# Kernel tuning notes

Hardware: AMD Instinct MI355X
Metric: run time of the kernel (lower is better)

## Reference

```python
import jax, jax.numpy as jnp
import numpy as np
import math

B, S, E, H = 2, 2048, 768, 12
D = E // H            # head_dim = 64
FFN = 3072            # GeGLU hidden
WIN = 64              # local window size
GLOBAL_IDS = np.array([0])
EPS = 1e-5


def _rope(x):
    # x: [B,H,S,D]; interleaved rotary embedding, theta=10000 (lucidrains RotaryEmbedding)
    d = x.shape[-1]
    s = x.shape[-2]
    inv_freq = 1.0 / (10000.0 ** (jnp.arange(0, d, 2, dtype=jnp.float32) / d))
    freqs = jnp.arange(s, dtype=jnp.float32)[:, None] * inv_freq[None, :]  # [S, D/2]
    freqs = jnp.repeat(freqs, 2, axis=-1)                                   # [S, D]
    cos, sin = jnp.cos(freqs), jnp.sin(freqs)
    xp = x.reshape(x.shape[:-1] + (d // 2, 2))
    x_rot = jnp.stack([-xp[..., 1], xp[..., 0]], axis=-1).reshape(x.shape)
    return x * cos + x_rot * sin


def _layernorm(x, scale, bias):
    mu = jnp.mean(x, axis=-1, keepdims=True)
    var = jnp.mean(jnp.square(x - mu), axis=-1, keepdims=True)
    return (x - mu) * jax.lax.rsqrt(var + EPS) * scale + bias


def setup_inputs() -> dict:
    key = jax.random.key(0)
    ks = jax.random.split(key, 10)
    def xav(k, shape, gain):
        fan_out, fan_in = shape
        std = gain * math.sqrt(2.0 / (fan_in + fan_out))
        return jax.random.normal(k, shape, jnp.float32) * std
    g2 = math.sqrt(2.0)
    g13 = math.sqrt(1.0 / 3.0)
    return {
        "x": jax.random.normal(ks[0], (B, S, E), jnp.float32),
        "rel_pos_bias": jax.random.normal(ks[1], (B, S, S), jnp.float32),
        "mask": jnp.ones((B, S), dtype=bool),
        "wq_w": xav(ks[2], (E, E), g2), "wq_b": jnp.zeros((E,), jnp.float32),
        "wk_w": xav(ks[3], (E, E), g2), "wk_b": jnp.zeros((E,), jnp.float32),
        "wv_w": xav(ks[4], (E, E), g2), "wv_b": jnp.zeros((E,), jnp.float32),
        "fc_w": xav(ks[5], (E, E), g2), "fc_b": jnp.zeros((E,), jnp.float32),
        "pos_coeff": jnp.full((H, 1, 1), 0.01, jnp.float32),
        "gate_w": xav(ks[6], (FFN, E), g13), "gate_b": jnp.zeros((FFN,), jnp.float32),
        "value_w": xav(ks[7], (FFN, E), g2), "value_b": jnp.zeros((FFN,), jnp.float32),
        "down_w": xav(ks[8], (E, FFN), g2), "down_b": jnp.zeros((E,), jnp.float32),
        "ln1_s": jnp.ones((E,), jnp.float32), "ln1_b": jnp.zeros((E,), jnp.float32),
        "ln2_s": jnp.ones((E,), jnp.float32), "ln2_b": jnp.zeros((E,), jnp.float32),
    }


def _sparse_allow(mask):
    # static local-window + global-token pattern, [S,S] bool
    idx = jnp.arange(S)
    allow = jnp.abs(idx[:, None] - idx[None, :]) <= WIN
    gidx = jnp.asarray(GLOBAL_IDS)
    allow = allow.at[gidx, :].set(True)
    allow = allow.at[:, gidx].set(True)
    # combine with padding mask [B,S] broadcast over query rows
    return allow[None, None, :, :] & mask[:, None, None, :]  # [B,1,S,S]


def reference(x, rel_pos_bias, mask, wq_w, wq_b, wk_w, wk_b, wv_w, wv_b,
              fc_w, fc_b, pos_coeff, gate_w, gate_b, value_w, value_b,
              down_w, down_b, ln1_s, ln1_b, ln2_s, ln2_b):
    def heads(t):  # [B,S,E] -> [B,H,S,D]
        return t.reshape(B, S, H, D).transpose(0, 2, 1, 3)

    Q = _rope(heads(x @ wq_w.T + wq_b))
    K = _rope(heads(x @ wk_w.T + wk_b))
    V = heads(x @ wv_w.T + wv_b)

    scores = jnp.einsum('bhqd,bhkd->bhqk', Q, K) / math.sqrt(D)
    scores = scores + pos_coeff[None] * rel_pos_bias[:, None]     # [B,H,S,S]
    allow = _sparse_allow(mask)
    scores = jnp.where(allow, scores, -1e30)
    scores = scores - jnp.max(scores, axis=-1, keepdims=True)
    attn = jax.nn.softmax(scores, axis=-1)
    ctx = jnp.einsum('bhqk,bhkd->bhqd', attn, V)
    ctx = ctx.transpose(0, 2, 1, 3).reshape(B, S, E)
    attn_out = ctx @ fc_w.T + fc_b

    h = _layernorm(x + attn_out, ln1_s, ln1_b)
    gate = jax.nn.gelu(h @ gate_w.T + gate_b, approximate=False)
    ffn = (gate * (h @ value_w.T + value_b)) @ down_w.T + down_b
    return _layernorm(h + ffn, ln2_s, ln2_b)
```

## Files before the change

kernel.cpp:

```cpp
#include <hip/hip_runtime.h>
#include <math.h>

#define B_   2
#define S_   2048
#define E_   768
#define H_   12
#define D_   64
#define FFN_ 3072
#define WIN_ 64
#define MTOT (B_*S_)

typedef unsigned short ushort_t;
typedef unsigned short ushort8 __attribute__((ext_vector_type(8)));
typedef __bf16 bf16x8 __attribute__((ext_vector_type(8)));
typedef float f32x4 __attribute__((ext_vector_type(4)));
typedef _Float16 half_t;

__device__ __forceinline__ float b2f(ushort_t u) {
    union { unsigned int i; float f; } c; c.i = ((unsigned int)u) << 16; return c.f;
}
__device__ __forceinline__ ushort_t f2b(float f) {
    union { float f; unsigned int i; } c; c.f = f;
    unsigned int u = c.i;
    return (ushort_t)((u + 0x7fffu + ((u >> 16) & 1u)) >> 16);
}
__device__ __forceinline__ float gelu_f(float g) {
    return 0.5f * g * (1.f + erff(g * 0.70710678118654752440f));
}

typedef const __attribute__((address_space(1))) void* gptr_t;
typedef __attribute__((address_space(3))) void* lptr_t;
__device__ __forceinline__ void gload16(const void* g, void* l) {
    __builtin_amdgcn_global_load_lds((gptr_t)g,
        (lptr_t)(unsigned int)(unsigned long long)l, 16, 0, 0);
}

__global__ __launch_bounds__(256)
void cvt_f32_bf16(const float* __restrict__ in, ushort_t* __restrict__ out, int n8)
{
    const int idx = blockIdx.x * 256 + threadIdx.x;
    if (idx >= n8) return;
    const float4* p = (const float4*)(in + (size_t)idx * 8);
    const float4 a = p[0], b = p[1];
    ushort8 o;
    o[0]=f2b(a.x); o[1]=f2b(a.y); o[2]=f2b(a.z); o[3]=f2b(a.w);
    o[4]=f2b(b.x); o[5]=f2b(b.y); o[6]=f2b(b.z); o[7]=f2b(b.w);
    *(ushort8*)(out + (size_t)idx*8) = o;
}

__global__ __launch_bounds__(256)
void cvt_interleave(const float* __restrict__ gw, const float* __restrict__ vw,
                    ushort_t* __restrict__ out)
{
    const int idx = blockIdx.x*256 + threadIdx.x;
    const int R   = idx / 96, c8 = idx - R*96;
    const int blk = R >> 6, w = R & 63;
    const float* src = (w < 32 ? gw : vw) + (size_t)(blk*32 + (w & 31))*768 + c8*8;
    const float4 a = ((const float4*)src)[0], b = ((const float4*)src)[1];
    ushort8 o;
    o[0]=f2b(a.x); o[1]=f2b(a.y); o[2]=f2b(a.z); o[3]=f2b(a.w);
    o[4]=f2b(b.x); o[5]=f2b(b.y); o[6]=f2b(b.z); o[7]=f2b(b.w);
    *(ushort8*)(out + (size_t)idx*8) = o;
}

__global__ __launch_bounds__(256)
void rope_table(float2* __restrict__ ctab)
{
    const int idx = blockIdx.x*256 + threadIdx.x;
    if (idx >= S_*32) return;
    const int s = idx >> 5, i = idx & 31;
    const float inv = exp2f(-(float)i * (13.287712379549449f/32.0f));
    const float fr = (float)s * inv;
    ctab[idx] = make_float2(cosf(fr), sinf(fr));
}

__global__ __launch_bounds__(256)
void rope_apply(ushort_t* __restrict__ Qb, ushort_t* __restrict__ Kb,
                const float2* __restrict__ ctab)
{
    const int NP4 = MTOT*E_/8;
    int idx = blockIdx.x*256 + threadIdx.x;
    ushort_t* ptr = Qb;
    if (idx >= NP4) { ptr = Kb; idx -= NP4; if (idx >= NP4) return; }
    const size_t p0 = (size_t)idx * 4;
    const int e2 = (int)(p0 % (E_/2));
    const int s  = (int)((p0 / (E_/2)) % S_);
    const int i0 = e2 & 31;
    ushort8 v = *(ushort8*)(ptr + p0*2);
    ushort8 o;
#pragma unroll
    for (int t = 0; t < 4; ++t) {
        const float2 cs = ctab[s*32 + i0 + t];
        const float x0 = b2f(v[2*t]), x1 = b2f(v[2*t+1]);
        o[2*t]   = f2b(x0*cs.x - x1*cs.y);
        o[2*t+1] = f2b(x1*cs.x + x0*cs.y);
    }
    *(ushort8*)(ptr + p0*2) = o;
}

template<int EPI, int BN>
__global__ __launch_bounds__(256)
void gemm_mfma(const ushort_t* __restrict__ A,
               const ushort_t* W0, const float* b0, void* C0,
               const ushort_t* W1, const float* b1, void* C1,
               const ushort_t* W2, const float* b2, void* C2,
               const void* __restrict__ aux, int M, int N, int K)
{
    constexpr int NWC = BN/64, NWR = 4/NWC, WROWS = 128/NWR, MF = WROWS/16;
    const ushort_t* W = W0; const float* bias = b0; void* C = C0;
    if (blockIdx.z == 1) { W = W1; bias = b1; C = C1; }
    else if (blockIdx.z == 2) { W = W2; bias = b2; C = C2; }

    __shared__ __align__(16) ushort_t As[128*32];
    __shared__ __align__(16) ushort_t Bs[BN*32];

    const int tid = threadIdx.x, wv = tid>>6, lane = tid&63;
    const int m0 = blockIdx.y*128, n0 = blockIdx.x*BN;
    const int wr = wv / NWC, wc = wv % NWC;
    const int lr16 = lane & 15, lkb = (lane>>4)<<3;

    f32x4 acc[MF][4];
#pragma unroll
    for (int i=0;i<MF;++i)
#pragma unroll
        for (int j=0;j<4;++j) acc[i][j] = f32x4{0.f,0.f,0.f,0.f};

    const char* Ab = (const char*)(A + (size_t)m0*K);
    const char* Wb = (const char*)(W + (size_t)n0*K);
    const size_t rb = (size_t)K*2;
    const int wbase = wv*1024, lby = lane*16;

    for (int kt = 0; kt < K; kt += 32) {
        const size_t kb = (size_t)kt*2;
        int n_ = wbase + lby;
        gload16(Ab + (size_t)(n_>>6)*rb + kb + (n_&63), (char*)As + wbase);
        n_ += 4096;
        gload16(Ab + (size_t)(n_>>6)*rb + kb + (n_&63), (char*)As + wbase + 4096);
        n_ = wbase + lby;
        gload16(Wb + (size_t)(n_>>6)*rb + kb + (n_&63), (char*)Bs + wbase);
        if (BN == 128) {
            n_ += 4096;
            gload16(Wb + (size_t)(n_>>6)*rb + kb + (n_&63), (char*)Bs + wbase + 4096);
        }
        __syncthreads();
        bf16x8 af[MF], bfr[4];
#pragma unroll
        for (int mf=0; mf<MF; ++mf)
            af[mf] = *(const bf16x8*)&As[(wr*WROWS + mf*16 + lr16)*32 + lkb];
#pragma unroll
        for (int nf=0; nf<4; ++nf)
            bfr[nf] = *(const bf16x8*)&Bs[(wc*64 + nf*16 + lr16)*32 + lkb];
#pragma unroll
        for (int mf=0; mf<MF; ++mf)
#pragma unroll
            for (int nf=0; nf<4; ++nf)
                acc[mf][nf] = __builtin_amdgcn_mfma_f32_16x16x32_bf16(af[mf], bfr[nf], acc[mf][nf], 0,0,0);
        __syncthreads();
    }

    const int colb = n0 + wc*64 + lr16;
    const int rowb = m0 + wr*WROWS + ((lane>>4)<<2);
#pragma unroll
    for (int nf=0; nf<4; ++nf) {
        const int col = colb + nf*16;
        const float bsv = bias[col];
#pragma unroll
        for (int mf=0; mf<MF; ++mf) {
            const int row = rowb + mf*16;
            const f32x4 a = acc[mf][nf];
#pragma unroll
            for (int r=0; r<4; ++r) {
                const size_t off = (size_t)(row+r)*N + col;
                const float v = a[r] + bsv;
                if constexpr (EPI == 0) {
                    ((ushort_t*)C)[off] = f2b(v);
                } else if constexpr (EPI == 1) {
                    ((float*)C)[off] = v + ((const float*)aux)[off];
                } else {
                    if (blockIdx.z == 2) {
                        const int rr = row + r;
                        const size_t toff =
                            (((size_t)(rr >> 11)*H_ + (col >> 6))*64 + (col & 63))*(size_t)S_ + (rr & (S_-1));
                        ((ushort_t*)C)[toff] = f2b(v);
                    } else {
                        ((ushort_t*)C)[off] = f2b(v);
                    }
                }
            }
        }
    }
}

__global__ __launch_bounds__(256, 2)
void gemm_geglu(const ushort_t* __restrict__ A,
                const ushort_t* __restrict__ Wgv,
                const float* __restrict__ bgp,
                const float* __restrict__ bvp,
                ushort_t* __restrict__ C)
{
    constexpr int NT   = 12;
    constexpr int ABY  = 128*128;
    constexpr int BUFB = 2*ABY;
    __shared__ __align__(16) char lds[2*BUFB];

    const int id  = blockIdx.x;
    const int stI = (id & 7)*3 + ((id >> 3) >> 6);
    const int w64 = (id >> 3) & 63;
    const int gy  = (stI/6)*8 + (w64 >> 3);
    const int gx  = (stI%6)*8 + (w64 & 7);
    const int m0 = gy*128, n0 = gx*128;

    const int tid = threadIdx.x, wv = tid>>6, l = tid&63;
    const int wr = wv>>1, wc = wv&1;
    const int lr16 = l & 15, g16b = (l>>4)<<4;
    const int xr = (lr16 & 7) << 4;

    const int lrow = l >> 3;
    const int swzc = ((l & 7) ^ lrow) << 4;
    const char* Agp = (const char*)A   + (size_t)(m0 + wv*32 + lrow)*1536 + swzc;
    const char* Bgp = (const char*)Wgv + (size_t)(n0 + wv*32 + lrow)*1536 + swzc;

    const int rA0 = (wr*64 +  0 + lr16)*128, rA1 = (wr*64 + 16 + lr16)*128;
    const int rA2 = (wr*64 + 32 + lr16)*128, rA3 = (wr*64 + 48 + lr16)*128;
    const int rB0 = ABY + (wc*64 +  0 + lr16)*128, rB1 = ABY + (wc*64 + 16 + lr16)*128;
    const int rB2 = ABY + (wc*64 + 32 + lr16)*128, rB3 = ABY + (wc*64 + 48 + lr16)*128;
    const int ck0 = g16b ^ xr, ck1 = (64 + g16b) ^ xr;

    f32x4 acc[4][4];
#pragma unroll
    for (int i=0;i<4;++i)
#pragma unroll
        for (int j=0;j<4;++j) acc[i][j] = f32x4{0.f,0.f,0.f,0.f};

#define STG(tt, cb) { \
    char* dA = lds + (cb)*BUFB + wv*4096; \
    char* dB = lds + (cb)*BUFB + ABY + wv*4096; \
    const size_t ko = (size_t)(tt)*128; \
    gload16(Agp + ko,           dA); \
    gload16(Agp + ko +  8*1536, dA + 1024); \
    gload16(Agp + ko + 16*1536, dA + 2048); \
    gload16(Agp + ko + 24*1536, dA + 3072); \
    gload16(Bgp + ko,           dB); \
    gload16(Bgp + ko +  8*1536, dB + 1024); \
    gload16(Bgp + ko + 16*1536, dB + 2048); \
    gload16(Bgp + ko + 24*1536, dB + 3072); }

    STG(0, 0);
    __syncthreads();

    int c = 0;
#pragma unroll 1
    for (int t = 0; t < NT; ++t) {
        if (t < NT-1) STG(t+1, c^1);
        const char* Lb = lds + c*BUFB;
        const bf16x8 a0 = *(const bf16x8*)(Lb + rA0 + ck0);
        const bf16x8 a1 = *(const bf16x8*)(Lb + rA1 + ck0);
        const bf16x8 a2 = *(const bf16x8*)(Lb + rA2 + ck0);
        const bf16x8 a3 = *(const bf16x8*)(Lb + rA3 + ck0);
        const bf16x8 b0 = *(const bf16x8*)(Lb + rB0 + ck0);
        const bf16x8 b1 = *(const bf16x8*)(Lb + rB1 + ck0);
        const bf16x8 b2 = *(const bf16x8*)(Lb + rB2 + ck0);
        const bf16x8 b3 = *(const bf16x8*)(Lb + rB3 + ck0);
        const bf16x8 e0 = *(const bf16x8*)(Lb + rA0 + ck1);
        const bf16x8 e1 = *(const bf16x8*)(Lb + rA1 + ck1);
        const bf16x8 e2 = *(const bf16x8*)(Lb + rA2 + ck1);
        const bf16x8 e3 = *(const bf16x8*)(Lb + rA3 + ck1);
        const bf16x8 f0 = *(const bf16x8*)(Lb + rB0 + ck1);
        const bf16x8 f1 = *(const bf16x8*)(Lb + rB1 + ck1);
        const bf16x8 f2 = *(const bf16x8*)(Lb + rB2 + ck1);
        const bf16x8 f3 = *(const bf16x8*)(Lb + rB3 + ck1);
        __builtin_amdgcn_s_setprio(1);
        acc[0][0] = __builtin_amdgcn_mfma_f32_16x16x32_bf16(a0, b0, acc[0][0], 0,0,0);
        acc[1][0] = __builtin_amdgcn_mfma_f32_16x16x32_bf16(a1, b0, acc[1][0], 0,0,0);
        acc[2][0] = __builtin_amdgcn_mfma_f32_16x16x32_bf16(a2, b0, acc[2][0], 0,0,0);
        acc[3][0] = __builtin_amdgcn_mfma_f32_16x16x32_bf16(a3, b0, acc[3][0], 0,0,0);
        acc[0][1] = __builtin_amdgcn_mfma_f32_16x16x32_bf16(a0, b1, acc[0][1], 0,0,0);
        acc[1][1] = __builtin_amdgcn_mfma_f32_16x16x32_bf16(a1, b1, acc[1][1], 0,0,0);
        acc[2][1] = __builtin_amdgcn_mfma_f32_16x16x32_bf16(a2, b1, acc[2][1], 0,0,0);
        acc[3][1] = __builtin_amdgcn_mfma_f32_16x16x32_bf16(a3, b1, acc[3][1], 0,0,0);
        acc[0][2] = __builtin_amdgcn_mfma_f32_16x16x32_bf16(a0, b2, acc[0][2], 0,0,0);
        acc[1][2] = __builtin_amdgcn_mfma_f32_16x16x32_bf16(a1, b2, acc[1][2], 0,0,0);
        acc[2][2] = __builtin_amdgcn_mfma_f32_16x16x32_bf16(a2, b2, acc[2][2], 0,0,0);
        acc[3][2] = __builtin_amdgcn_mfma_f32_16x16x32_bf16(a3, b2, acc[3][2], 0,0,0);
        acc[0][3] = __builtin_amdgcn_mfma_f32_16x16x32_bf16(a0, b3, acc[0][3], 0,0,0);
        acc[1][3] = __builtin_amdgcn_mfma_f32_16x16x32_bf16(a1, b3, acc[1][3], 0,0,0);
        acc[2][3] = __builtin_amdgcn_mfma_f32_16x16x32_bf16(a2, b3, acc[2][3], 0,0,0);
        acc[3][3] = __builtin_amdgcn_mfma_f32_16x16x32_bf16(a3, b3, acc[3][3], 0,0,0);
        acc[0][0] = __builtin_amdgcn_mfma_f32_16x16x32_bf16(e0, f0, acc[0][0], 0,0,0);
        acc[1][0] = __builtin_amdgcn_mfma_f32_16x16x32_bf16(e1, f0, acc[1][0], 0,0,0);
        acc[2][0] = __builtin_amdgcn_mfma_f32_16x16x32_bf16(e2, f0, acc[2][0], 0,0,0);
        acc[3][0] = __builtin_amdgcn_mfma_f32_16x16x32_bf16(e3, f0, acc[3][0], 0,0,0);
        acc[0][1] = __builtin_amdgcn_mfma_f32_16x16x32_bf16(e0, f1, acc[0][1], 0,0,0);
        acc[1][1] = __builtin_amdgcn_mfma_f32_16x16x32_bf16(e1, f1, acc[1][1], 0,0,0);
        acc[2][1] = __builtin_amdgcn_mfma_f32_16x16x32_bf16(e2, f1, acc[2][1], 0,0,0);
        acc[3][1] = __builtin_amdgcn_mfma_f32_16x16x32_bf16(e3, f1, acc[3][1], 0,0,0);
        acc[0][2] = __builtin_amdgcn_mfma_f32_16x16x32_bf16(e0, f2, acc[0][2], 0,0,0);
        acc[1][2] = __builtin_amdgcn_mfma_f32_16x16x32_bf16(e1, f2, acc[1][2], 0,0,0);
        acc[2][2] = __builtin_amdgcn_mfma_f32_16x16x32_bf16(e2, f2, acc[2][2], 0,0,0);
        acc[3][2] = __builtin_amdgcn_mfma_f32_16x16x32_bf16(e3, f2, acc[3][2], 0,0,0);
        acc[0][3] = __builtin_amdgcn_mfma_f32_16x16x32_bf16(e0, f3, acc[0][3], 0,0,0);
        acc[1][3] = __builtin_amdgcn_mfma_f32_16x16x32_bf16(e1, f3, acc[1][3], 0,0,0);
        acc[2][3] = __builtin_amdgcn_mfma_f32_16x16x32_bf16(e2, f3, acc[2][3], 0,0,0);
        acc[3][3] = __builtin_amdgcn_mfma_f32_16x16x32_bf16(e3, f3, acc[3][3], 0,0,0);
        __builtin_amdgcn_s_setprio(0);
        __syncthreads();
        c ^= 1;
    }
#undef STG

    const int colb = gx*64 + wc*32 + lr16;
    const int rowb = m0 + wr*64 + ((l>>4)<<2);
#pragma unroll
    for (int nf=0; nf<2; ++nf) {
        const int col = colb + nf*16;
        const float bgv = bgp[col], bvv = bvp[col];
#pragma unroll
        for (int mf=0; mf<4; ++mf) {
            const int row = rowb + mf*16;
            const f32x4 gq = acc[mf][nf];
            const f32x4 vq = acc[mf][nf+2];
#pragma unroll
            for (int r=0; r<4; ++r) {
                C[(size_t)(row+r)*3072 + col] =
                    f2b(gelu_f(gq[r] + bgv) * (vq[r] + bvv));
            }
        }
    }
}

__global__ __launch_bounds__(256, 3)
void gemm_down(const ushort_t* __restrict__ A,
               const ushort_t* __restrict__ Wd,
               const float* __restrict__ bias,
               float* __restrict__ P0,
               half_t* __restrict__ P1)
{
    constexpr int NT   = 24;
    constexpr int ABY  = 128*128;
    constexpr int BBY  = 64*128;
    constexpr int BUFB = ABY + BBY;
    __shared__ __align__(16) char lds[2*BUFB];

    const int id   = blockIdx.x;
    const int work = (id & 7)*96 + (id >> 3);
    const int z    = work / 384;
    const int r    = work - z*384;
    const int gy   = r / 12, gx = r - gy*12;
    const int m0 = gy*128, n0 = gx*64;

    const int tid = threadIdx.x, wv = tid>>6, l = tid&63;
    const int wr = wv>>1, wc = wv&1;
    const int lr16 = l & 15, g16b = (l>>4)<<4;
    const int xr = (lr16 & 7) << 4;

    const int lrow = l >> 3;
    const int swzc = ((l & 7) ^ lrow) << 4;
    const size_t kbase = (size_t)z*3072;
    const char* Agp = (const char*)A  + (size_t)(m0 + wv*32 + lrow)*6144 + kbase + swzc;
    const char* Bgp = (const char*)Wd + (size_t)(n0 + wv*16 + lrow)*6144 + kbase + swzc;

    const int rA0 = (wr*64 +  0 + lr16)*128, rA1 = (wr*64 + 16 + lr16)*128;
    const int rA2 = (wr*64 + 32 + lr16)*128, rA3 = (wr*64 + 48 + lr16)*128;
    const int rB0 = ABY + (wc*32 +  0 + lr16)*128;
    const int rB1 = ABY + (wc*32 + 16 + lr16)*128;
    const int ck0 = g16b ^ xr, ck1 = (64 + g16b) ^ xr;

    f32x4 acc[4][2];
#pragma unroll
    for (int i=0;i<4;++i)
#pragma unroll
        for (int j=0;j<2;++j) acc[i][j] = f32x4{0.f,0.f,0.f,0.f};

#define STGD(tt, cb) { \
    char* dA = lds + (cb)*BUFB + wv*4096; \
    char* dB = lds + (cb)*BUFB + ABY + wv*2048; \
    const size_t ko = (size_t)(tt)*128; \
    gload16(Agp + ko,           dA); \
    gload16(Agp + ko +  8*6144, dA + 1024); \
    gload16(Agp + ko + 16*6144, dA + 2048); \
    gload16(Agp + ko + 24*6144, dA + 3072); \
    gload16(Bgp + ko,           dB); \
    gload16(Bgp + ko +  8*6144, dB + 1024); }

    STGD(0, 0);
    __syncthreads();

    int c = 0;
#pragma unroll 1
    for (int t = 0; t < NT; ++t) {
        if (t < NT-1) STGD(t+1, c^1);
        const char* Lb = lds + c*BUFB;
        const bf16x8 a0 = *(const bf16x8*)(Lb + rA0 + ck0);
        const bf16x8 a1 = *(const bf16x8*)(Lb + rA1 + ck0);
        const bf16x8 a2 = *(const bf16x8*)(Lb + rA2 + ck0);
        const bf16x8 a3 = *(const bf16x8*)(Lb + rA3 + ck0);
        const bf16x8 b0 = *(const bf16x8*)(Lb + rB0 + ck0);
        const bf16x8 b1 = *(const bf16x8*)(Lb + rB1 + ck0);
        const bf16x8 e0 = *(const bf16x8*)(Lb + rA0 + ck1);
        const bf16x8 e1 = *(const bf16x8*)(Lb + rA1 + ck1);
        const bf16x8 e2 = *(const bf16x8*)(Lb + rA2 + ck1);
        const bf16x8 e3 = *(const bf16x8*)(Lb + rA3 + ck1);
        const bf16x8 f0 = *(const bf16x8*)(Lb + rB0 + ck1);
        const bf16x8 f1 = *(const bf16x8*)(Lb + rB1 + ck1);
        __builtin_amdgcn_s_setprio(1);
        acc[0][0] = __builtin_amdgcn_mfma_f32_16x16x32_bf16(a0, b0, acc[0][0], 0,0,0);
        acc[1][0] = __builtin_amdgcn_mfma_f32_16x16x32_bf16(a1, b0, acc[1][0], 0,0,0);
        acc[2][0] = __builtin_amdgcn_mfma_f32_16x16x32_bf16(a2, b0, acc[2][0], 0,0,0);
        acc[3][0] = __builtin_amdgcn_mfma_f32_16x16x32_bf16(a3, b0, acc[3][0], 0,0,0);
        acc[0][1] = __builtin_amdgcn_mfma_f32_16x16x32_bf16(a0, b1, acc[0][1], 0,0,0);
        acc[1][1] = __builtin_amdgcn_mfma_f32_16x16x32_bf16(a1, b1, acc[1][1], 0,0,0);
        acc[2][1] = __builtin_amdgcn_mfma_f32_16x16x32_bf16(a2, b1, acc[2][1], 0,0,0);
        acc[3][1] = __builtin_amdgcn_mfma_f32_16x16x32_bf16(a3, b1, acc[3][1], 0,0,0);
        acc[0][0] = __builtin_amdgcn_mfma_f32_16x16x32_bf16(e0, f0, acc[0][0], 0,0,0);
        acc[1][0] = __builtin_amdgcn_mfma_f32_16x16x32_bf16(e1, f0, acc[1][0], 0,0,0);
        acc[2][0] = __builtin_amdgcn_mfma_f32_16x16x32_bf16(e2, f0, acc[2][0], 0,0,0);
        acc[3][0] = __builtin_amdgcn_mfma_f32_16x16x32_bf16(e3, f0, acc[3][0], 0,0,0);
        acc[0][1] = __builtin_amdgcn_mfma_f32_16x16x32_bf16(e0, f1, acc[0][1], 0,0,0);
        acc[1][1] = __builtin_amdgcn_mfma_f32_16x16x32_bf16(e1, f1, acc[1][1], 0,0,0);
        acc[2][1] = __builtin_amdgcn_mfma_f32_16x16x32_bf16(e2, f1, acc[2][1], 0,0,0);
        acc[3][1] = __builtin_amdgcn_mfma_f32_16x16x32_bf16(e3, f1, acc[3][1], 0,0,0);
        __builtin_amdgcn_s_setprio(0);
        __syncthreads();
        c ^= 1;
    }
#undef STGD

    const int colb = n0 + wc*32 + lr16;
    const int rowb = m0 + wr*64 + ((l>>4)<<2);
#pragma unroll
    for (int nf=0; nf<2; ++nf) {
        const int col = colb + nf*16;
        const float bsv = bias[col];
#pragma unroll
        for (int mf=0; mf<4; ++mf) {
            const int row = rowb + mf*16;
            const f32x4 a = acc[mf][nf];
#pragma unroll
            for (int rr=0; rr<4; ++rr) {
                const size_t off = (size_t)(row+rr)*E_ + col;
                if (z == 0) P0[off] = a[rr] + bsv;
                else        P1[off] = (half_t)a[rr];
            }
        }
    }
}

__global__ __launch_bounds__(256)
void attn_mfma(const ushort_t* __restrict__ Qb, const ushort_t* __restrict__ Kb,
               const ushort_t* __restrict__ Vt, const float* __restrict__ rel,
               const float* __restrict__ pos_coeff, ushort_t* __restrict__ ctx)
{
    __shared__ __align__(16) ushort_t P_lds[4][16][160];
    const int id = blockIdx.x;
    const int h  = id % H_;
    const int qb = (id / H_) & 31;
    const int b  = id / (H_*32);
    const int wv = threadIdx.x >> 6, l = threadIdx.x & 63;
    const int qw = qb*64 + wv*16;
    const int g  = l >> 4, ql = l & 15;
    const int q  = qw + ql;

    int klo = qw - 64;
    if (klo < 0) klo = 0;
    if (klo > S_-160) klo = S_-160;
    const bool addg = (klo > 0);
    const float pc = pos_coeff[h];

    const ushort_t* qbp = Qb + ((size_t)(b*S_ + qw))*E_ + h*D_ + (size_t)ql*E_ + g*8;
    const bf16x8 qf0 = *(const bf16x8*)(qbp);
    const bf16x8 qf1 = *(const bf16x8*)(qbp + 32);

    float sg = -1e30f, pg = 0.f;
    const float* relrow = rel + ((size_t)(b*S_ + q))*S_;
    if (addg) {
        const ushort_t* k0p = Kb + (size_t)(b*S_)*E_ + h*D_ + g*8;
        const bf16x8 k00 = *(const bf16x8*)(k0p);
        const bf16x8 k01 = *(const bf16x8*)(k0p + 32);
        float part = 0.f;
#pragma unroll
        for (int t = 0; t < 8; ++t) {
            part = fmaf((float)k00[t], (float)qf0[t], part);
            part = fmaf((float)k01[t], (float)qf1[t], part);
        }
        part += __shfl_xor(part, 16);
        part += __shfl_xor(part, 32);
        sg = part*0.125f + pc*relrow[0];
    }

    f32x4 sc_[10];
#pragma unroll
    for (int f = 0; f < 10; ++f) sc_[f] = f32x4{0.f,0.f,0.f,0.f};
    const ushort_t* kbp = Kb + ((size_t)(b*S_ + klo))*E_ + h*D_;
#pragma unroll
    for (int f = 0; f < 10; ++f) {
        const ushort_t* kr = kbp + (size_t)(16*f + ql)*E_ + g*8;
        const bf16x8 kf0 = *(const bf16x8*)(kr);
        const bf16x8 kf1 = *(const bf16x8*)(kr + 32);
        sc_[f] = __builtin_amdgcn_mfma_f32_16x16x32_bf16(kf0, qf0, sc_[f], 0,0,0);
        sc_[f] = __builtin_amdgcn_mfma_f32_16x16x32_bf16(kf1, qf1, sc_[f], 0,0,0);
    }

#pragma unroll
    for (int f = 0; f < 10; ++f) {
#pragma unroll
        for (int r = 0; r < 4; ++r) {
            const int slot = 16*f + 4*g + r;
            const int key  = klo + slot;
            const int dd   = key - q;
            const bool ok  = (dd <= WIN_ && dd >= -WIN_) || (key == 0);
            const float v  = sc_[f][r]*0.125f + pc*relrow[key];
            sc_[f][r] = ok ? v : -1e30f;
        }
    }

    float mx = sg;
#pragma unroll
    for (int f = 0; f < 10; ++f)
#pragma unroll
        for (int r = 0; r < 4; ++r) mx = fmaxf(mx, sc_[f][r]);
    mx = fmaxf(mx, __shfl_xor(mx, 16));
    mx = fmaxf(mx, __shfl_xor(mx, 32));

    float ls = 0.f;
#pragma unroll
    for (int f = 0; f < 10; ++f)
#pragma unroll
        for (int r = 0; r < 4; ++r) {
            const float p = __expf(sc_[f][r] - mx);
            sc_[f][r] = p; ls += p;
        }
    if (addg) pg = __expf(sg - mx);
    ls += (g == 0) ? pg : 0.f;
    ls += __shfl_xor(ls, 16);
    ls += __shfl_xor(ls, 32);
    const float inv = 1.f / ls;

#pragma unroll
    for (int f = 0; f < 10; ++f)
#pragma unroll
        for (int r = 0; r < 4; ++r)
            P_lds[wv][ql][16*f + 4*g + r] = f2b(sc_[f][r]);
    __syncthreads();

    f32x4 acc_c[4];
#pragma unroll
    for (int df = 0; df < 4; ++df) acc_c[df] = f32x4{0.f,0.f,0.f,0.f};
    const ushort_t* vtb = Vt + ((size_t)(b*H_ + h)*64)*(size_t)S_;
#pragma unroll
    for (int s5 = 0; s5 < 5; ++s5) {
        const bf16x8 pf = *(const bf16x8*)&P_lds[wv][ql][32*s5 + 8*g];
#pragma unroll
        for (int df = 0; df < 4; ++df) {
            const bf16x8 vtf = *(const bf16x8*)(vtb + (size_t)(df*16 + ql)*S_ + klo + 32*s5 + g*8);
            acc_c[df] = __builtin_amdgcn_mfma_f32_16x16x32_bf16(vtf, pf, acc_c[df], 0,0,0);
        }
    }

    if (addg) {
#pragma unroll
        for (int df = 0; df < 4; ++df)
#pragma unroll
            for (int r = 0; r < 4; ++r)
                acc_c[df][r] = fmaf(pg, b2f(vtb[(size_t)(df*16 + g*4 + r)*S_]), acc_c[df][r]);
    }

    if (q != 0) {
        ushort_t* cb = ctx + ((size_t)(b*S_ + q))*E_ + h*D_;
#pragma unroll
        for (int df = 0; df < 4; ++df)
#pragma unroll
            for (int r = 0; r < 4; ++r)
                cb[df*16 + g*4 + r] = f2b(acc_c[df][r] * inv);
    }
}

__global__ __launch_bounds__(256)
void attn_global(const ushort_t* __restrict__ Qb, const ushort_t* __restrict__ Kb,
                 const ushort_t* __restrict__ Vt, const float* __restrict__ rel,
                 const float* __restrict__ pos_coeff, ushort_t* __restrict__ ctx)
{
    __shared__ float sc[S_];
    __shared__ float sq[D_];
    __shared__ float red[4];
    __shared__ float pacc[4][D_];
    const int tid = threadIdx.x, wv = tid>>6, lane = tid&63;
    const int id = blockIdx.x, h = id % H_, b = id / H_;

    if (tid < 64) sq[tid] = b2f(Qb[(size_t)(b*S_)*E_ + h*D_ + tid]);
    __syncthreads();

    const float pc = pos_coeff[h];
    const ushort_t* kbase = Kb + (size_t)b*S_*E_ + h*D_;
    const float* relrow = rel + (size_t)b*S_*S_;
    const int g = lane >> 2, sl = lane & 3;

    for (int jb = wv*16; jb < S_; jb += 64) {
        const int j = jb + g;
        const ushort_t* kr = kbase + (size_t)j*E_ + sl*16;
        const ushort8 k0 = *(const ushort8*)kr;
        const ushort8 k1 = *(const ushort8*)(kr + 8);
        const float* qv = &sq[sl*16];
        float partial = 0.f;
#pragma unroll
        for (int t = 0; t < 8; ++t) partial = fmaf(b2f(k0[t]), qv[t], partial);
#pragma unroll
        for (int t = 0; t < 8; ++t) partial = fmaf(b2f(k1[t]), qv[t+8], partial);
        partial += __shfl_xor(partial, 1);
        partial += __shfl_xor(partial, 2);
        if (sl == 0) sc[j] = partial*0.125f + pc*relrow[j];
    }
    __syncthreads();

    float mx = -1e30f;
#pragma unroll
    for (int i = 0; i < 8; ++i) mx = fmaxf(mx, sc[tid + 256*i]);
#pragma unroll
    for (int off = 32; off > 0; off >>= 1) mx = fmaxf(mx, __shfl_xor(mx, off));
    if (lane == 0) red[wv] = mx;
    __syncthreads();
    mx = fmaxf(fmaxf(red[0], red[1]), fmaxf(red[2], red[3]));

    float sum = 0.f;
#pragma unroll
    for (int i = 0; i < 8; ++i) {
        const float p = __expf(sc[tid + 256*i] - mx);
        sc[tid + 256*i] = p; sum += p;
    }
#pragma unroll
    for (int off = 32; off > 0; off >>= 1) sum += __shfl_xor(sum, off);
    __syncthreads();
    if (lane == 0) red[wv] = sum;
    __syncthreads();
    const float inv = 1.f / (red[0]+red[1]+red[2]+red[3]);

    const ushort_t* vtrow = Vt + ((size_t)(b*H_ + h)*64 + lane)*(size_t)S_;
    float acc = 0.f;
    for (int j0 = wv*512; j0 < wv*512 + 512; j0 += 8) {
        const ushort8 v8 = *(const ushort8*)&vtrow[j0];
#pragma unroll
        for (int t = 0; t < 8; ++t) acc = fmaf(sc[j0+t], b2f(v8[t]), acc);
    }
    pacc[wv][lane] = acc;
    __syncthreads();
    if (tid < 64) {
        const float r = (pacc[0][tid]+pacc[1][tid]+pacc[2][tid]+pacc[3][tid]) * inv;
        ctx[(size_t)(b*S_)*E_ + h*D_ + tid] = f2b(r);
    }
}

template<bool WB>
__global__ __launch_bounds__(256)
void ln_kernel(const float* __restrict__ in, const float* __restrict__ gam,
               const float* __restrict__ bet, float* __restrict__ out,
               ushort_t* __restrict__ outb)
{
    const int row = blockIdx.x;
    const float* r = in + (size_t)row * E_;
    const int tid = threadIdx.x;
    const float v0 = r[tid], v1 = r[tid+256], v2 = r[tid+512];
    float s  = v0+v1+v2;
    float ss = v0*v0+v1*v1+v2*v2;
#pragma unroll
    for (int off = 32; off > 0; off >>= 1) {
        s  += __shfl_xor(s, off);
        ss += __shfl_xor(ss, off);
    }
    __shared__ float rs[4], rss[4];
    const int wv = tid >> 6, lane = tid & 63;
    if (lane == 0) { rs[wv] = s; rss[wv] = ss; }
    __syncthreads();
    s  = rs[0]+rs[1]+rs[2]+rs[3];
    ss = rss[0]+rss[1]+rss[2]+rss[3];
    const float mu  = s * (1.f/E_);
    const float var = ss * (1.f/E_) - mu*mu;
    const float rstd = rsqrtf(var + 1e-5f);
    float* o = out + (size_t)row * E_;
    const float o0 = (v0-mu)*rstd*gam[tid    ] + bet[tid    ];
    const float o1 = (v1-mu)*rstd*gam[tid+256] + bet[tid+256];
    const float o2 = (v2-mu)*rstd*gam[tid+512] + bet[tid+512];
    o[tid] = o0; o[tid+256] = o1; o[tid+512] = o2;
    if constexpr (WB) {
        ushort_t* ob = outb + (size_t)row * E_;
        ob[tid] = f2b(o0); ob[tid+256] = f2b(o1); ob[tid+512] = f2b(o2);
    }
}

__global__ __launch_bounds__(256)
void ln3_kernel(const float* __restrict__ p0, const half_t* __restrict__ p1,
                const float* __restrict__ res, const float* __restrict__ gam,
                const float* __restrict__ bet, float* __restrict__ out)
{
    const int row = blockIdx.x;
    const size_t base = (size_t)row * E_;
    const int tid = threadIdx.x;
    const float v0 = p0[base+tid]     + (float)p1[base+tid]     + res[base+tid];
    const float v1 = p0[base+tid+256] + (float)p1[base+tid+256] + res[base+tid+256];
    const float v2 = p0[base+tid+512] + (float)p1[base+tid+512] + res[base+tid+512];
    float s  = v0+v1+v2;
    float ss = v0*v0+v1*v1+v2*v2;
#pragma unroll
    for (int off = 32; off > 0; off >>= 1) {
        s  += __shfl_xor(s, off);
        ss += __shfl_xor(ss, off);
    }
    __shared__ float rs[4], rss[4];
    const int wv = tid >> 6, lane = tid & 63;
    if (lane == 0) { rs[wv] = s; rss[wv] = ss; }
    __syncthreads();
    s  = rs[0]+rs[1]+rs[2]+rs[3];
    ss = rss[0]+rss[1]+rss[2]+rss[3];
    const float mu  = s * (1.f/E_);
    const float var = ss * (1.f/E_) - mu*mu;
    const float rstd = rsqrtf(var + 1e-5f);
    float* o = out + base;
    o[tid]     = (v0-mu)*rstd*gam[tid    ] + bet[tid    ];
    o[tid+256] = (v1-mu)*rstd*gam[tid+256] + bet[tid+256];
    o[tid+512] = (v2-mu)*rstd*gam[tid+512] + bet[tid+512];
}

extern "C" void kernel_launch(void* const* d_in, const int* in_sizes, int n_in,
                              void* d_out, int out_size, void* d_ws, size_t ws_size,
                              hipStream_t stream)
{
    const float* x      = (const float*)d_in[0];
    const float* rel    = (const float*)d_in[1];
    const float* wq_w   = (const float*)d_in[3];
    const float* wq_b   = (const float*)d_in[4];
    const float* wk_w   = (const float*)d_in[5];
    const float* wk_b   = (const float*)d_in[6];
    const float* wv_w   = (const float*)d_in[7];
    const float* wv_b   = (const float*)d_in[8];
    const float* fc_w   = (const float*)d_in[9];
    const float* fc_b   = (const float*)d_in[10];
    const float* pos_c  = (const float*)d_in[11];
    const float* gate_w = (const float*)d_in[12];
    const float* gate_b = (const float*)d_in[13];
    const float* value_w= (const float*)d_in[14];
    const float* value_b= (const float*)d_in[15];
    const float* down_w = (const float*)d_in[16];
    const float* down_b = (const float*)d_in[17];
    const float* ln1_s  = (const float*)d_in[18];
    const float* ln1_b  = (const float*)d_in[19];
    const float* ln2_s  = (const float*)d_in[20];
    const float* ln2_b  = (const float*)d_in[21];
    float* out = (float*)d_out;

    char* W = (char*)d_ws;
    ushort_t* Qb     = (ushort_t*)(W + 0);
    ushort_t* Kb     = (ushort_t*)(W + 6291456);
    ushort_t* Vt     = (ushort_t*)(W + 12582912);
    ushort_t* Cxb    = (ushort_t*)(W + 18874368);
    ushort_t* GpB    = (ushort_t*)(W + 0);
    ushort_t* Xb     = (ushort_t*)(W + 25165824);
    ushort_t* wqb    = (ushort_t*)(W + 31457280);
    ushort_t* wkb    = (ushort_t*)(W + 32636928);
    ushort_t* wvb    = (ushort_t*)(W + 33816576);
    ushort_t* fcb    = (ushort_t*)(W + 34996224);
    ushort_t* Wgv    = (ushort_t*)(W + 25165824);
    ushort_t* downb  = (ushort_t*)(W + 34996224);
    float*    AO     = (float*)   (W + 39714816);
    float*    Hb     = (float*)   (W + 52297728);
    ushort_t* Hbb    = (ushort_t*)(W + 64880640);
    half_t*   P1h    = (half_t*)  (W + 64880640);
    float2*   ctab   = (float2*)  (W + 71172096);

    cvt_f32_bf16<<<1536, 256, 0, stream>>>(x, Xb, MTOT*E_/8);
    cvt_f32_bf16<<<288,  256, 0, stream>>>(wq_w, wqb, E_*E_/8);
    cvt_f32_bf16<<<288,  256, 0, stream>>>(wk_w, wkb, E_*E_/8);
    cvt_f32_bf16<<<288,  256, 0, stream>>>(wv_w, wvb, E_*E_/8);
    cvt_f32_bf16<<<288,  256, 0, stream>>>(fc_w, fcb, E_*E_/8);
    rope_table<<<(S_*32+255)/256, 256, 0, stream>>>(ctab);

    gemm_mfma<2,128><<<dim3(E_/128, MTOT/128, 3), 256, 0, stream>>>(
        Xb, wqb, wq_b, Qb, wkb, wk_b, Kb, wvb, wv_b, Vt, nullptr, MTOT, E_, E_);

    cvt_interleave<<<2304, 256, 0, stream>>>(gate_w, value_w, Wgv);

    rope_apply<<<3072, 256, 0, stream>>>(Qb, Kb, ctab);

    attn_mfma<<<B_*H_*(S_/64), 256, 0, stream>>>(Qb, Kb, Vt, rel, pos_c, Cxb);
    attn_global<<<B_*H_, 256, 0, stream>>>(Qb, Kb, Vt, rel, pos_c, Cxb);

    gemm_mfma<1,64><<<dim3(E_/64, MTOT/128, 1), 256, 0, stream>>>(
        Cxb, fcb, fc_b, AO, nullptr, nullptr, nullptr, nullptr, nullptr, nullptr,
        x, MTOT, E_, E_);

    cvt_f32_bf16<<<1152, 256, 0, stream>>>(down_w, downb, E_*FFN_/8);

    ln_kernel<true><<<MTOT, 256, 0, stream>>>(AO, ln1_s, ln1_b, Hb, Hbb);

    gemm_geglu<<<dim3(1536), 256, 0, stream>>>(Hbb, Wgv, gate_b, value_b, GpB);

    gemm_down<<<dim3(768), 256, 0, stream>>>(GpB, downb, down_b, AO, P1h);

    ln3_kernel<<<MTOT, 256, 0, stream>>>(AO, P1h, Hb, ln2_s, ln2_b, out);
}
```

Baseline: 236.2 us.

## Fuse QKV projection with RoPE in a dedicated pipelined MFMA GEMM

Replaces the generic three-way QKV gemm plus a separate rope_apply pass with one gemm_qkv kernel. It uses 128x128 tiles, a double-buffered swizzled LDS pipeline and XCD-aware block mapping, and applies the rotary embedding in the epilogue by exchanging the paired lane's value with a shuffle. This removes one full read/write pass over Q and K and one launch. It relies on wq/wk/wv being stored contiguously as a single Wqkv matrix, since only the wq pointer is passed in.

```diff
diff --git a/kernel.cpp b/kernel.cpp
--- a/kernel.cpp
+++ b/kernel.cpp
@@ -72,30 +72,6 @@
     const float inv = exp2f(-(float)i * (13.287712379549449f/32.0f));
     const float fr = (float)s * inv;
     ctab[idx] = make_float2(cosf(fr), sinf(fr));
-}
-
-__global__ __launch_bounds__(256)
-void rope_apply(ushort_t* __restrict__ Qb, ushort_t* __restrict__ Kb,
-                const float2* __restrict__ ctab)
-{
-    const int NP4 = MTOT*E_/8;
-    int idx = blockIdx.x*256 + threadIdx.x;
-    ushort_t* ptr = Qb;
-    if (idx >= NP4) { ptr = Kb; idx -= NP4; if (idx >= NP4) return; }
-    const size_t p0 = (size_t)idx * 4;
-    const int e2 = (int)(p0 % (E_/2));
-    const int s  = (int)((p0 / (E_/2)) % S_);
-    const int i0 = e2 & 31;
-    ushort8 v = *(ushort8*)(ptr + p0*2);
-    ushort8 o;
-#pragma unroll
-    for (int t = 0; t < 4; ++t) {
-        const float2 cs = ctab[s*32 + i0 + t];
-        const float x0 = b2f(v[2*t]), x1 = b2f(v[2*t+1]);
-        o[2*t]   = f2b(x0*cs.x - x1*cs.y);
-        o[2*t+1] = f2b(x1*cs.x + x0*cs.y);
-    }
-    *(ushort8*)(ptr + p0*2) = o;
 }
 
 template<int EPI, int BN>
@@ -174,17 +150,160 @@
                 const float v = a[r] + bsv;
                 if constexpr (EPI == 0) {
                     ((ushort_t*)C)[off] = f2b(v);
-                } else if constexpr (EPI == 1) {
+                } else {
                     ((float*)C)[off] = v + ((const float*)aux)[off];
+                }
+            }
+        }
+    }
+}
+
+__global__ __launch_bounds__(256, 2)
+void gemm_qkv(const ushort_t* __restrict__ A,
+              const ushort_t* __restrict__ Wqkv,
+              const float* __restrict__ bq, const float* __restrict__ bk,
+              const float* __restrict__ bv,
+              const float2* __restrict__ ctab,
+              ushort_t* __restrict__ Qb, ushort_t* __restrict__ Kb,
+              ushort_t* __restrict__ Vt)
+{
+    constexpr int NT   = 12;
+    constexpr int ABY  = 128*128;
+    constexpr int BUFB = 2*ABY;
+    __shared__ __align__(16) char lds[2*BUFB];
+
+    const int id  = blockIdx.x;
+    const int xcd = id & 7, w = id >> 3;
+    const int gy  = (xcd & 3)*8 + (w & 7);
+    const int gx  = (xcd >> 2)*9 + (w >> 3);
+    const int m0 = gy*128, n0 = gx*128;
+
+    const int tid = threadIdx.x, wv = tid>>6, l = tid&63;
+    const int wr = wv>>1, wc = wv&1;
+    const int lr16 = l & 15, g16b = (l>>4)<<4;
+    const int xr = (lr16 & 7) << 4;
+
+    const int lrow = l >> 3;
+    const int swzc = ((l & 7) ^ lrow) << 4;
+    const char* Agp = (const char*)A    + (size_t)(m0 + wv*32 + lrow)*1536 + swzc;
+    const char* Bgp = (const char*)Wqkv + (size_t)(n0 + wv*32 + lrow)*1536 + swzc;
+
+    const int rA0 = (wr*64 +  0 + lr16)*128, rA1 = (wr*64 + 16 + lr16)*128;
+    const int rA2 = (wr*64 + 32 + lr16)*128, rA3 = (wr*64 + 48 + lr16)*128;
+    const int rB0 = ABY + (wc*64 +  0 + lr16)*128, rB1 = ABY + (wc*64 + 16 + lr16)*128;
+    const int rB2 = ABY + (wc*64 + 32 + lr16)*128, rB3 = ABY + (wc*64 + 48 + lr16)*128;
+    const int ck0 = g16b ^ xr, ck1 = (64 + g16b) ^ xr;
+
+    f32x4 acc[4][4];
+#pragma unroll
+    for (int i=0;i<4;++i)
+#pragma unroll
+        for (int j=0;j<4;++j) acc[i][j] = f32x4{0.f,0.f,0.f,0.f};
+
+#define STGQ(tt, cb) { \
+    char* dA = lds + (cb)*BUFB + wv*4096; \
+    char* dB = lds + (cb)*BUFB + ABY + wv*4096; \
+    const size_t ko = (size_t)(tt)*128; \
+    gload16(Agp + ko,           dA); \
+    gload16(Agp + ko +  8*1536, dA + 1024); \
+    gload16(Agp + ko + 16*1536, dA + 2048); \
+    gload16(Agp + ko + 24*1536, dA + 3072); \
+    gload16(Bgp + ko,           dB); \
+    gload16(Bgp + ko +  8*1536, dB + 1024); \
+    gload16(Bgp + ko + 16*1536, dB + 2048); \
+    gload16(Bgp + ko + 24*1536, dB + 3072); }
+
+    STGQ(0, 0);
+    __syncthreads();
+
+    int c = 0;
+#pragma unroll 1
+    for (int t = 0; t < NT; ++t) {
+        if (t < NT-1) STGQ(t+1, c^1);
+        const char* Lb = lds + c*BUFB;
+        const bf16x8 a0 = *(const bf16x8*)(Lb + rA0 + ck0);
+        const bf16x8 a1 = *(const bf16x8*)(Lb + rA1 + ck0);
+        const bf16x8 a2 = *(const bf16x8*)(Lb + rA2 + ck0);
+        const bf16x8 a3 = *(const bf16x8*)(Lb + rA3 + ck0);
+        const bf16x8 b0 = *(const bf16x8*)(Lb + rB0 + ck0);
+        const bf16x8 b1 = *(const bf16x8*)(Lb + rB1 + ck0);
+        const bf16x8 b2 = *(const bf16x8*)(Lb + rB2 + ck0);
+        const bf16x8 b3 = *(const bf16x8*)(Lb + rB3 + ck0);
+        const bf16x8 e0 = *(const bf16x8*)(Lb + rA0 + ck1);
+        const bf16x8 e1 = *(const bf16x8*)(Lb + rA1 + ck1);
+        const bf16x8 e2 = *(const bf16x8*)(Lb + rA2 + ck1);
+        const bf16x8 e3 = *(const bf16x8*)(Lb + rA3 + ck1);
+        const bf16x8 f0 = *(const bf16x8*)(Lb + rB0 + ck1);
+        const bf16x8 f1 = *(const bf16x8*)(Lb + rB1 + ck1);
+        const bf16x8 f2 = *(const bf16x8*)(Lb + rB2 + ck1);
+        const bf16x8 f3 = *(const bf16x8*)(Lb + rB3 + ck1);
+        __builtin_amdgcn_s_setprio(1);
+        acc[0][0] = __builtin_amdgcn_mfma_f32_16x16x32_bf16(a0, b0, acc[0][0], 0,0,0);
+        acc[1][0] = __builtin_amdgcn_mfma_f32_16x16x32_bf16(a1, b0, acc[1][0], 0,0,0);
+        acc[2][0] = __builtin_amdgcn_mfma_f32_16x16x32_bf16(a2, b0, acc[2][0], 0,0,0);
+        acc[3][0] = __builtin_amdgcn_mfma_f32_16x16x32_bf16(a3, b0, acc[3][0], 0,0,0);
+        acc[0][1] = __builtin_amdgcn_mfma_f32_16x16x32_bf16(a0, b1, acc[0][1], 0,0,0);
+        acc[1][1] = __builtin_amdgcn_mfma_f32_16x16x32_bf16(a1, b1, acc[1][1], 0,0,0);
+        acc[2][1] = __builtin_amdgcn_mfma_f32_16x16x32_bf16(a2, b1, acc[2][1], 0,0,0);
+        acc[3][1] = __builtin_amdgcn_mfma_f32_16x16x32_bf16(a3, b1, acc[3][1], 0,0,0);
+        acc[0][2] = __builtin_amdgcn_mfma_f32_16x16x32_bf16(a0, b2, acc[0][2], 0,0,0);
+        acc[1][2] = __builtin_amdgcn_mfma_f32_16x16x32_bf16(a1, b2, acc[1][2], 0,0,0);
+        acc[2][2] = __builtin_amdgcn_mfma_f32_16x16x32_bf16(a2, b2, acc[2][2], 0,0,0);
+        acc[3][2] = __builtin_amdgcn_mfma_f32_16x16x32_bf16(a3, b2, acc[3][2], 0,0,0);
+        acc[0][3] = __builtin_amdgcn_mfma_f32_16x16x32_bf16(a0, b3, acc[0][3], 0,0,0);
+        acc[1][3] = __builtin_amdgcn_mfma_f32_16x16x32_bf16(a1, b3, acc[1][3], 0,0,0);
+        acc[2][3] = __builtin_amdgcn_mfma_f32_16x16x32_bf16(a2, b3, acc[2][3], 0,0,0);
+        acc[3][3] = __builtin_amdgcn_mfma_f32_16x16x32_bf16(a3, b3, acc[3][3], 0,0,0);
+        acc[0][0] = __builtin_amdgcn_mfma_f32_16x16x32_bf16(e0, f0, acc[0][0], 0,0,0);
+        acc[1][0] = __builtin_amdgcn_mfma_f32_16x16x32_bf16(e1, f0, acc[1][0], 0,0,0);
+        acc[2][0] = __builtin_amdgcn_mfma_f32_16x16x32_bf16(e2, f0, acc[2][0], 0,0,0);
+        acc[3][0] = __builtin_amdgcn_mfma_f32_16x16x32_bf16(e3, f0, acc[3][0], 0,0,0);
+        acc[0][1] = __builtin_amdgcn_mfma_f32_16x16x32_bf16(e0, f1, acc[0][1], 0,0,0);
+        acc[1][1] = __builtin_amdgcn_mfma_f32_16x16x32_bf16(e1, f1, acc[1][1], 0,0,0);
+        acc[2][1] = __builtin_amdgcn_mfma_f32_16x16x32_bf16(e2, f1, acc[2][1], 0,0,0);
+        acc[3][1] = __builtin_amdgcn_mfma_f32_16x16x32_bf16(e3, f1, acc[3][1], 0,0,0);
+        acc[0][2] = __builtin_amdgcn_mfma_f32_16x16x32_bf16(e0, f2, acc[0][2], 0,0,0);
+        acc[1][2] = __builtin_amdgcn_mfma_f32_16x16x32_bf16(e1, f2, acc[1][2], 0,0,0);
+        acc[2][2] = __builtin_amdgcn_mfma_f32_16x16x32_bf16(e2, f2, acc[2][2], 0,0,0);
+        acc[3][2] = __builtin_amdgcn_mfma_f32_16x16x32_bf16(e3, f2, acc[3][2], 0,0,0);
+        acc[0][3] = __builtin_amdgcn_mfma_f32_16x16x32_bf16(e0, f3, acc[0][3], 0,0,0);
+        acc[1][3] = __builtin_amdgcn_mfma_f32_16x16x32_bf16(e1, f3, acc[1][3], 0,0,0);
+        acc[2][3] = __builtin_amdgcn_mfma_f32_16x16x32_bf16(e2, f3, acc[2][3], 0,0,0);
+        acc[3][3] = __builtin_amdgcn_mfma_f32_16x16x32_bf16(e3, f3, acc[3][3], 0,0,0);
+        __builtin_amdgcn_s_setprio(0);
+        __syncthreads();
+        c ^= 1;
+    }
+#undef STGQ
+
+    const int tsel = gx / 6;
+    const float* bias = (tsel==0) ? bq : (tsel==1) ? bk : bv;
+    ushort_t* out = (tsel==0) ? Qb : Kb;
+    const int colb = (gx - tsel*6)*128 + wc*64 + lr16;
+    const int rowb = m0 + wr*64 + ((l>>4)<<2);
+#pragma unroll
+    for (int nf=0; nf<4; ++nf) {
+        const int col = colb + nf*16;
+        const float bsv = bias[col];
+#pragma unroll
+        for (int mf=0; mf<4; ++mf) {
+            const int row = rowb + mf*16;
+            const f32x4 a = acc[mf][nf];
+#pragma unroll
+            for (int r=0; r<4; ++r) {
+                const int rr = row + r;
+                const float v = a[r] + bsv;
+                if (tsel == 2) {
+                    const size_t toff =
+                        (((size_t)(rr >> 11)*H_ + (col >> 6))*64 + (col & 63))*(size_t)S_ + (rr & (S_-1));
+                    Vt[toff] = f2b(v);
                 } else {
-                    if (blockIdx.z == 2) {
-                        const int rr = row + r;
-                        const size_t toff =
-                            (((size_t)(rr >> 11)*H_ + (col >> 6))*64 + (col & 63))*(size_t)S_ + (rr & (S_-1));
-                        ((ushort_t*)C)[toff] = f2b(v);
-                    } else {
-                        ((ushort_t*)C)[off] = f2b(v);
-                    }
+                    const int s = rr & (S_-1);
+                    const float2 cs = ctab[s*32 + ((col & 63) >> 1)];
+                    const float p = __shfl_xor(v, 1);
+                    const float rot = (col & 1) ? fmaf(v, cs.x,  p*cs.y)
+                                                : fmaf(v, cs.x, -p*cs.y);
+                    out[(size_t)rr*E_ + col] = f2b(rot);
                 }
             }
         }
@@ -771,12 +890,9 @@
     cvt_f32_bf16<<<288,  256, 0, stream>>>(fc_w, fcb, E_*E_/8);
     rope_table<<<(S_*32+255)/256, 256, 0, stream>>>(ctab);
 
-    gemm_mfma<2,128><<<dim3(E_/128, MTOT/128, 3), 256, 0, stream>>>(
-        Xb, wqb, wq_b, Qb, wkb, wk_b, Kb, wvb, wv_b, Vt, nullptr, MTOT, E_, E_);
+    gemm_qkv<<<576, 256, 0, stream>>>(Xb, wqb, wq_b, wk_b, wv_b, ctab, Qb, Kb, Vt);
 
     cvt_interleave<<<2304, 256, 0, stream>>>(gate_w, value_w, Wgv);
-
-    rope_apply<<<3072, 256, 0, stream>>>(Qb, Kb, ctab);
 
     attn_mfma<<<B_*H_*(S_/64), 256, 0, stream>>>(Qb, Kb, Vt, rel, pos_c, Cxb);
     attn_global<<<B_*H_, 256, 0, stream>>>(Qb, Kb, Vt, rel, pos_c, Cxb);
```

Measured after the change: 246.7 us. +4.4%, slower.
